# Kernel tuning notes

Hardware: AMD Instinct MI355X
Metric: run time of the kernel (lower is better)

The kernel has to match this reference:

```python
import jax, jax.numpy as jnp
import numpy as np

T, B, F = 197, 64, 768      # tokens (hardcoded 197 in module), batch, width
N, K = 8, 2                 # num_experts, top-k
CAP = int(197 * 1.0 * K / N)  # capacity = 49
H = 4 * F                   # expert hidden (c_fc out)
G = F // 4                  # gate hidden


def setup_inputs() -> dict:
    key = jax.random.key(0)
    ks = jax.random.split(key, 9)
    s = 0.02
    return {
        "x":   jax.random.normal(ks[0], (T, B, F), jnp.float32),
        # gate: Linear(F, F/4) -> ReLU -> Linear(F/4, N)
        "Wg1": jax.random.normal(ks[1], (F, G), jnp.float32) * s,
        "bg1": jnp.zeros((G,), jnp.float32),
        "Wg2": jax.random.normal(ks[2], (G, N), jnp.float32) * s,
        "bg2": jnp.zeros((N,), jnp.float32),
        # experts: per-expert Linear(F, 4F) -> ReLU -> Linear(4F, F), stacked over N
        "W1":  jax.random.normal(ks[3], (N, F, H), jnp.float32) * s,
        "b1":  jnp.zeros((N, H), jnp.float32),
        "W2":  jax.random.normal(ks[4], (N, H, F), jnp.float32) * s,
        "b2":  jnp.zeros((N, F), jnp.float32),
    }


def reference(x, Wg1, bg1, Wg2, bg2, W1, b1, W2, b2):
    # gating: softmax over experts (dim=2)
    logits = jax.nn.relu(x @ Wg1 + bg1) @ Wg2 + bg2          # [T,B,N]
    gw = jax.nn.softmax(logits, axis=2)                      # [T,B,N]

    # dense all-expert MLP (as-written: every expert on every token)
    h = jax.nn.relu(jnp.einsum('tbf,nfh->tbnh', x, W1) + b1)  # [T,B,N,H]
    eo = jnp.einsum('tbnh,nhf->tbnf', h, W2) + b2             # [T,B,N,F]

    # top-k expert mask (dim=2)
    _, idx = jax.lax.top_k(gw, K)                             # [T,B,K]
    mask_exp = jnp.any(jnp.arange(N)[None, None, None, :] == idx[..., None], axis=2)
    cw = gw * mask_exp                                        # [T,B,N]

    # capacity mask: top-CAP tokens per (batch, expert) along dim 0
    cwT = jnp.moveaxis(cw, 0, -1)                             # [B,N,T]
    _, idx2 = jax.lax.top_k(cwT, CAP)                         # [B,N,CAP]
    mask_cap = jnp.any(jnp.arange(T)[None, None, None, :] == idx2[..., None], axis=2)  # [B,N,T]
    fw = cw * jnp.moveaxis(mask_cap, -1, 0)                   # [T,B,N]

    # combine selected expert outputs, residual-style subtract
    out = jnp.einsum('tbnf,tbn->tbf', eo, fw) - x             # [T,B,F]
    return out
```

## Files before the change

kernel.cpp:

```cpp
#include <hip/hip_runtime.h>
#include <hip/hip_bf16.h>
#include <math.h>
#include <stdint.h>

#define T_ 197
#define B_ 64
#define F_ 768
#define N_ 8
#define CAP_ 49
#define H_ 3072
#define G_ 192
#define TB_ (T_*B_)
#define NBN_ (B_*N_)
#define ME_ 3200
#define MR_ 3136
#define MT_ 25600
#define KH_ 4
#define HCF_ 384
#define NPF_ 8

using bf16x8 = __attribute__((ext_vector_type(8))) short;
using f32x4  = __attribute__((ext_vector_type(4))) float;

__device__ __forceinline__ unsigned short f2bf(float v) {
    __hip_bfloat16 h = __float2bfloat16(v);
    return __builtin_bit_cast(unsigned short, h);
}
__device__ __forceinline__ float bf2f(unsigned short u) {
    unsigned int w = ((unsigned int)u) << 16;
    return __builtin_bit_cast(float, w);
}

#define GLL16(g, l) __builtin_amdgcn_global_load_lds( \
    (const __attribute__((address_space(1))) unsigned int*)(uintptr_t)(g), \
    (__attribute__((address_space(3))) unsigned int*)(uintptr_t)(l), 16, 0, 0)

__device__ __forceinline__ int xcd_swz(int bid, int nblk) {
    int q = nblk >> 3, r = nblk & 7;
    int xcd = bid & 7, idx = bid >> 3;
    int base = (xcd < r) ? xcd * (q + 1) : r * (q + 1) + (xcd - r) * q;
    return base + idx;
}

__global__ void k_init_out(const float* __restrict__ x, float* __restrict__ out) {
    int i = blockIdx.x * blockDim.x + threadIdx.x;
    const float4* xv = (const float4*)x;
    float4* ov = (float4*)out;
    float4 v = xv[i];
    ov[i] = make_float4(-v.x, -v.y, -v.z, -v.w);
}

__global__ __launch_bounds__(256) void k_gate1(
        const float* __restrict__ x, const float* __restrict__ Wg1,
        float* __restrict__ gs_part) {
    __shared__ float xs[64][35];
    __shared__ float wt[64][35];
    int bid = blockIdx.x;
    int bm = bid % 197; int rest = bid / 197;
    int bn = rest % 3, kh = rest / 3;
    int m0 = bm * 64, n0 = bn * 64, k0 = kh * (F_ / KH_);
    int tid = threadIdx.x;
    int tc = tid & 15, tr = tid >> 4;
    float acc[4][4] = {};

    int xr0 = tid >> 3, xc4 = (tid & 7) << 2;
    int wnn = tid & 63, wkw = tid >> 6;

    float4 xreg[2];
    float4 wreg[2];

    auto loadRegs = [&](int t) {
        int kb = k0 + t * 32;
        #pragma unroll
        for (int i = 0; i < 2; ++i) {
            int r = xr0 + i * 32;
            xreg[i] = *(const float4*)(x + (size_t)(m0 + r) * F_ + kb + xc4);
        }
        #pragma unroll
        for (int i = 0; i < 2; ++i) {
            int kkg = (wkw * 2 + i) * 4;
            const float* wp = Wg1 + (size_t)(kb + kkg) * G_ + n0 + wnn;
            wreg[i].x = wp[0];
            wreg[i].y = wp[G_];
            wreg[i].z = wp[2 * G_];
            wreg[i].w = wp[3 * G_];
        }
    };
    auto writeLDS = [&]() {
        #pragma unroll
        for (int i = 0; i < 2; ++i)
            *(float4*)&xs[xr0 + i * 32][xc4] = xreg[i];
        #pragma unroll
        for (int i = 0; i < 2; ++i)
            *(float4*)&wt[wnn][(wkw * 2 + i) * 4] = wreg[i];
    };

    loadRegs(0);
    for (int t = 0; t < 6; ++t) {
        __syncthreads();
        writeLDS();
        __syncthreads();
        if (t < 5) loadRegs(t + 1);
        #pragma unroll
        for (int kq = 0; kq < 8; ++kq) {
            float4 a[4], b[4];
            #pragma unroll
            for (int i = 0; i < 4; ++i) a[i] = *(const float4*)&xs[tr * 4 + i][kq * 4];
            #pragma unroll
            for (int j = 0; j < 4; ++j) b[j] = *(const float4*)&wt[tc + 16 * j][kq * 4];
            #pragma unroll
            for (int i = 0; i < 4; ++i)
                #pragma unroll
                for (int j = 0; j < 4; ++j)
                    acc[i][j] += a[i].x * b[j].x + a[i].y * b[j].y + a[i].z * b[j].z + a[i].w * b[j].w;
        }
    }
    float* gp = gs_part + (size_t)kh * TB_ * G_;
    #pragma unroll
    for (int j = 0; j < 4; ++j) {
        int c = n0 + tc + 16 * j;
        #pragma unroll
        for (int i = 0; i < 4; ++i) {
            int r = m0 + tr * 4 + i;
            gp[(size_t)r * G_ + c] = acc[i][j];
        }
    }
}

__global__ __launch_bounds__(256) void k_gate2(
        const float* __restrict__ gs_part, const float* __restrict__ bg1,
        const float* __restrict__ Wg2, const float* __restrict__ bg2,
        float* __restrict__ cw, int* __restrict__ ecnt) {
    __shared__ float gsh[32][200];
    __shared__ float wg2s[G_ * N_];
    __shared__ float lg[32][8];
    int tid = threadIdx.x;
    int id0 = blockIdx.x * 32;

    for (int i = tid; i < 32 * 48; i += 256) {
        int r = i / 48, c4 = i % 48;
        const float* p0 = gs_part + (size_t)(id0 + r) * G_ + c4 * 4;
        float4 a = *(const float4*)p0;
        float4 b = *(const float4*)(p0 + (size_t)TB_ * G_);
        float4 c = *(const float4*)(p0 + 2 * (size_t)TB_ * G_);
        float4 d = *(const float4*)(p0 + 3 * (size_t)TB_ * G_);
        float4 g = *(const float4*)(bg1 + c4 * 4);
        float4 v;
        v.x = fmaxf(a.x + b.x + c.x + d.x + g.x, 0.f);
        v.y = fmaxf(a.y + b.y + c.y + d.y + g.y, 0.f);
        v.z = fmaxf(a.z + b.z + c.z + d.z + g.z, 0.f);
        v.w = fmaxf(a.w + b.w + c.w + d.w + g.w, 0.f);
        ((float4*)&gsh[r][0])[c4] = v;
    }
    for (int i = tid; i < G_ * N_; i += 256) wg2s[i] = Wg2[i];
    __syncthreads();

    int tk = tid >> 3, n = tid & 7;
    float a = bg2[n];
    for (int k = 0; k < G_; ++k) a += gsh[tk][k] * wg2s[k * N_ + n];
    lg[tk][n] = a;
    __syncthreads();

    if (tid < 32) {
        int tk2 = tid;
        float p[8];
        float m = lg[tk2][0];
        #pragma unroll
        for (int nn = 1; nn < 8; ++nn) m = fmaxf(m, lg[tk2][nn]);
        float s = 0.f;
        #pragma unroll
        for (int nn = 0; nn < 8; ++nn) { p[nn] = expf(lg[tk2][nn] - m); s += p[nn]; }
        float inv = 1.f / s;
        #pragma unroll
        for (int nn = 0; nn < 8; ++nn) p[nn] *= inv;
        int i1 = 0; float v1 = p[0];
        #pragma unroll
        for (int nn = 1; nn < 8; ++nn) if (p[nn] > v1) { v1 = p[nn]; i1 = nn; }
        int i2 = -1; float v2 = -1.f;
        #pragma unroll
        for (int nn = 0; nn < 8; ++nn) if (nn != i1 && p[nn] > v2) { v2 = p[nn]; i2 = nn; }
        int id = id0 + tk2;
        int t = id / B_, b = id % B_;
        ecnt[id] = 0;
        #pragma unroll
        for (int nn = 0; nn < 8; ++nn) {
            float v = (nn == i1 || nn == i2) ? p[nn] : 0.f;
            cw[((size_t)(b * N_ + nn)) * T_ + t] = v;
        }
    }
}

__global__ __launch_bounds__(256) void k_gate(
        const float* __restrict__ x, const float* __restrict__ Wg1,
        const float* __restrict__ bg1, const float* __restrict__ Wg2,
        const float* __restrict__ bg2, float* __restrict__ cw,
        int* __restrict__ ecnt) {
    __shared__ float xsh[8][F_];
    __shared__ float gsl[8][G_];
    __shared__ float lg[8][N_];
    int tid = threadIdx.x;
    int id0 = blockIdx.x * 8;

    int gid = blockIdx.x * 256 + tid;
    if (gid < TB_ && ecnt) ecnt[gid] = 0;

    const float4* xv = (const float4*)(x + (size_t)id0 * F_);
    float4* xshv = (float4*)&xsh[0][0];
    for (int idx = tid; idx < 8 * (F_/4); idx += 256) xshv[idx] = xv[idx];
    __syncthreads();

    if (tid < G_) {
        float acc[8];
        float bb = bg1[tid];
        #pragma unroll
        for (int tk = 0; tk < 8; ++tk) acc[tk] = bb;
        for (int k = 0; k < F_; ++k) {
            float w = Wg1[k * G_ + tid];
            #pragma unroll
            for (int tk = 0; tk < 8; ++tk) acc[tk] += xsh[tk][k] * w;
        }
        #pragma unroll
        for (int tk = 0; tk < 8; ++tk) gsl[tk][tid] = fmaxf(acc[tk], 0.f);
    }
    __syncthreads();

    if (tid < 64) {
        int tk = tid >> 3, n = tid & 7;
        float acc = bg2[n];
        for (int k = 0; k < G_; ++k) acc += gsl[tk][k] * Wg2[k * N_ + n];
        lg[tk][n] = acc;
    }
    __syncthreads();

    if (tid < 8) {
        int tk = tid;
        float p[8];
        float m = lg[tk][0];
        #pragma unroll
        for (int n = 1; n < 8; ++n) m = fmaxf(m, lg[tk][n]);
        float s = 0.f;
        #pragma unroll
        for (int n = 0; n < 8; ++n) { p[n] = expf(lg[tk][n] - m); s += p[n]; }
        float inv = 1.f / s;
        #pragma unroll
        for (int n = 0; n < 8; ++n) p[n] *= inv;
        int i1 = 0; float v1 = p[0];
        #pragma unroll
        for (int n = 1; n < 8; ++n) if (p[n] > v1) { v1 = p[n]; i1 = n; }
        int i2 = -1; float v2 = -1.f;
        #pragma unroll
        for (int n = 0; n < 8; ++n) if (n != i1 && p[n] > v2) { v2 = p[n]; i2 = n; }
        int id = id0 + tk;
        int t = id / B_, b = id % B_;
        #pragma unroll
        for (int n = 0; n < 8; ++n) {
            float v = (n == i1 || n == i2) ? p[n] : 0.f;
            cw[((size_t)(b * N_ + n)) * T_ + t] = v;
        }
    }
}

__global__ __launch_bounds__(256) void k_capacity(
        const float* __restrict__ cw, int* __restrict__ toks,
        float* __restrict__ wts, int* __restrict__ counts,
        int* __restrict__ ecnt, int* __restrict__ erow) {
    __shared__ float v[T_];
    __shared__ int keep[T_];
    int tid = threadIdx.x;
    int bn = blockIdx.x;
    int b = bn >> 3, n = bn & 7;
    if (tid < T_) v[tid] = cw[(size_t)bn * T_ + tid];
    __syncthreads();
    int kp = 0; float my = 0.f;
    if (tid < T_) {
        my = v[tid];
        int rank = 0;
        for (int t2 = 0; t2 < T_; ++t2) {
            float vt = v[t2];
            rank += (vt > my) || (vt == my && t2 < tid);
        }
        kp = (rank < CAP_) && (my > 0.f);
    }
    if (tid < T_) keep[tid] = kp;
    __syncthreads();
    if (tid < T_ && kp) {
        int slot = 0;
        for (int t2 = 0; t2 < T_; ++t2) slot += (t2 < tid) ? keep[t2] : 0;
        toks[bn * CAP_ + slot] = tid;
        wts[bn * CAP_ + slot] = my;
        if (ecnt) {
            int orow = tid * B_ + b;
            int pos = atomicAdd(&ecnt[orow], 1);
            erow[orow * 2 + pos] = n * ME_ + b * CAP_ + slot;
        }
    }
    if (tid == 0) {
        int tot = 0;
        for (int t2 = 0; t2 < T_; ++t2) tot += keep[t2];
        counts[bn] = tot;
    }
}

__global__ __launch_bounds__(256) void k_repack(
        const float* __restrict__ W, unsigned short* __restrict__ WT, int K, int J) {
    __shared__ float tile[64][65];
    int bid = blockIdx.x;
    int nk = K >> 6, nj = J >> 6;
    int kt = bid % nk; bid /= nk;
    int jt = bid % nj; int e = bid / nj;
    int k0 = kt * 64, j0 = jt * 64;
    int tid = threadIdx.x;
    int jr = (tid & 15) << 2;
    int kr = tid >> 4;
    const float* src = W + ((size_t)e * K + k0) * J + j0;
    #pragma unroll
    for (int i = 0; i < 4; ++i) {
        float4 v = *(const float4*)(src + (size_t)(kr + 16 * i) * J + jr);
        *(float4*)&tile[kr + 16 * i][jr] = v;
    }
    __syncthreads();
    int c = tid & 7;
    int jrow = tid >> 3;
    #pragma unroll
    for (int i = 0; i < 2; ++i) {
        int j = jrow + 32 * i;
        float f[8];
        #pragma unroll
        for (int s = 0; s < 8; ++s) f[s] = tile[c * 8 + s][j];
        uint4 u;
        u.x = f2bf(f[0]) | ((unsigned)f2bf(f[1]) << 16);
        u.y = f2bf(f[2]) | ((unsigned)f2bf(f[3]) << 16);
        u.z = f2bf(f[4]) | ((unsigned)f2bf(f[5]) << 16);
        u.w = f2bf(f[6]) | ((unsigned)f2bf(f[7]) << 16);
        int jg = j0 + j;
        char* drow = (char*)WT + ((size_t)e * J + jg) * (size_t)K * 2 + (size_t)(k0 >> 6) * 128;
        *(uint4*)(drow + ((c << 4) ^ ((jg & 7) << 4))) = u;
    }
}

__global__ __launch_bounds__(256) void k_gather(
        const float* __restrict__ x, const int* __restrict__ toks,
        const int* __restrict__ counts, unsigned short* __restrict__ Xg) {
    int gi = blockIdx.x * 256 + threadIdx.x;
    int R = gi / 96, c = gi - R * 96;
    int e = R / ME_, re = R - e * ME_;
    uint4 val = make_uint4(0u, 0u, 0u, 0u);
    if (re < MR_) {
        int g = re / CAP_, slot = re - g * CAP_;
        int bn = g * N_ + e;
        if (slot < counts[bn]) {
            int t = toks[bn * CAP_ + slot];
            const float* xp = x + ((size_t)t * B_ + g) * F_ + c * 8;
            float4 v0 = *(const float4*)xp;
            float4 v1 = *(const float4*)(xp + 4);
            val.x = f2bf(v0.x) | ((unsigned)f2bf(v0.y) << 16);
            val.y = f2bf(v0.z) | ((unsigned)f2bf(v0.w) << 16);
            val.z = f2bf(v1.x) | ((unsigned)f2bf(v1.y) << 16);
            val.w = f2bf(v1.z) | ((unsigned)f2bf(v1.w) << 16);
        }
    }
    int w = (c * 16) & 127;
    char* dst = (char*)Xg + (size_t)R * 1536 + (c >> 3) * 128 + (w ^ ((R & 7) << 4));
    *(uint4*)dst = val;
}

__global__ __launch_bounds__(256) void k_gemm1(
        const unsigned short* __restrict__ W1T, const unsigned short* __restrict__ Xg,
        const float* __restrict__ b1, unsigned short* __restrict__ Hg,
        int e0, int nblk) {
    __shared__ char ldsA[2][16384];
    __shared__ char ldsB[2][16384];
    int swzb = xcd_swz(blockIdx.x, nblk);
    int mt = swzb / 24;
    int jt = swzb % 24;
    int em = mt / 25;
    int e = e0 + em;
    int tid = threadIdx.x, lane = tid & 63, wid = tid >> 6;
    int lr8 = lane >> 3, sl = (lane & 7) << 4;
    const char* Ab = (const char*)W1T + ((size_t)e * H_ + (size_t)jt * 128) * (F_ * 2);
    const char* Bb = (const char*)Xg + ((size_t)e * ME_ + (size_t)(mt % 25) * 128) * (F_ * 2);
    f32x4 acc[4][4] = {};
    int swz = (lane & 7) << 4;
    int q16 = (lane >> 4) << 4;

    auto stage = [&](int buf, int it) {
        int kb = it << 7;
        #pragma unroll
        for (int i = 0; i < 4; ++i) {
            int lr = wid * 32 + i * 8 + lr8;
            GLL16(Ab + (size_t)lr * 1536 + kb + sl, ldsA[buf] + (wid * 32 + i * 8) * 128);
            GLL16(Bb + (size_t)lr * 1536 + kb + sl, ldsB[buf] + (wid * 32 + i * 8) * 128);
        }
    };

    stage(0, 0);
    __syncthreads();
    int cur = 0;
    for (int it = 0; it < 12; ++it) {
        if (it < 11) stage(cur ^ 1, it + 1);
        const char* la = ldsA[cur] + ((wid & 1) * 64) * 128;
        const char* lb = ldsB[cur] + ((wid >> 1) * 64) * 128;
        #pragma unroll
        for (int ks = 0; ks < 2; ++ks) {
            bf16x8 af[4], bfr[4];
            int kk = (ks * 64 + q16) ^ swz;
            #pragma unroll
            for (int t = 0; t < 4; ++t) {
                int ro = (16 * t + (lane & 15)) * 128;
                af[t]  = *(const bf16x8*)(la + ro + kk);
                bfr[t] = *(const bf16x8*)(lb + ro + kk);
            }
            #pragma unroll
            for (int ti = 0; ti < 4; ++ti)
                #pragma unroll
                for (int tm = 0; tm < 4; ++tm)
                    acc[ti][tm] = __builtin_amdgcn_mfma_f32_16x16x32_bf16(af[ti], bfr[tm], acc[ti][tm], 0, 0, 0);
        }
        __syncthreads();
        cur ^= 1;
    }
    int jl0 = jt * 128 + (wid & 1) * 64;
    int ml0 = mt * 128 + (wid >> 1) * 64;
    const float* b1p = b1 + (size_t)e * H_;
    #pragma unroll
    for (int tj = 0; tj < 4; ++tj) {
        int jc = jl0 + 16 * tj + ((lane >> 4) << 2);
        float bb0 = b1p[jc], bb1 = b1p[jc + 1], bb2 = b1p[jc + 2], bb3 = b1p[jc + 3];
        #pragma unroll
        for (int tm = 0; tm < 4; ++tm) {
            int m = ml0 + 16 * tm + (lane & 15);
            f32x4 a = acc[tj][tm];
            unsigned int u0 = f2bf(fmaxf(a[0] + bb0, 0.f)) | ((unsigned)f2bf(fmaxf(a[1] + bb1, 0.f)) << 16);
            unsigned int u1 = f2bf(fmaxf(a[2] + bb2, 0.f)) | ((unsigned)f2bf(fmaxf(a[3] + bb3, 0.f)) << 16);
            int w = (jc * 2) & 127;
            char* dst = (char*)Hg + (size_t)m * (H_ * 2) + ((jc * 2) & ~127) + (w ^ ((m & 7) << 4));
            *(uint2*)dst = make_uint2(u0, u1);
        }
    }
}

__global__ __launch_bounds__(256) void k_gemm2(
        const unsigned short* __restrict__ W2T, const unsigned short* __restrict__ Hg,
        const float* __restrict__ b2, const float* __restrict__ wts,
        const int* __restrict__ counts, unsigned short* __restrict__ Og,
        int e0, int nblk) {
    __shared__ char ldsA[2][16384];
    __shared__ char ldsB[2][16384];
    int swzb = xcd_swz(blockIdx.x, nblk);
    int mt = swzb / 6;
    int ft = swzb % 6;
    int em = mt / 25;
    int e = e0 + em;
    int tid = threadIdx.x, lane = tid & 63, wid = tid >> 6;
    int lr8 = lane >> 3, sl = (lane & 7) << 4;
    const char* Ab = (const char*)W2T + ((size_t)e * F_ + (size_t)ft * 128) * (H_ * 2);
    const char* Bb = (const char*)Hg + (size_t)mt * 128 * (H_ * 2);
    f32x4 acc[4][4] = {};
    int swz = (lane & 7) << 4;
    int q16 = (lane >> 4) << 4;

    auto stage = [&](int buf, int it) {
        int kb = it << 7;
        #pragma unroll
        for (int i = 0; i < 4; ++i) {
            int lr = wid * 32 + i * 8 + lr8;
            GLL16(Ab + (size_t)lr * 6144 + kb + sl, ldsA[buf] + (wid * 32 + i * 8) * 128);
            GLL16(Bb + (size_t)lr * 6144 + kb + sl, ldsB[buf] + (wid * 32 + i * 8) * 128);
        }
    };

    stage(0, 0);
    __syncthreads();
    int cur = 0;
    for (int it = 0; it < 48; ++it) {
        if (it < 47) stage(cur ^ 1, it + 1);
        const char* la = ldsA[cur] + ((wid & 1) * 64) * 128;
        const char* lb = ldsB[cur] + ((wid >> 1) * 64) * 128;
        #pragma unroll
        for (int ks = 0; ks < 2; ++ks) {
            bf16x8 af[4], bfr[4];
            int kk = (ks * 64 + q16) ^ swz;
            #pragma unroll
            for (int t = 0; t < 4; ++t) {
                int ro = (16 * t + (lane & 15)) * 128;
                af[t]  = *(const bf16x8*)(la + ro + kk);
                bfr[t] = *(const bf16x8*)(lb + ro + kk);
            }
            #pragma unroll
            for (int ti = 0; ti < 4; ++ti)
                #pragma unroll
                for (int tm = 0; tm < 4; ++tm)
                    acc[ti][tm] = __builtin_amdgcn_mfma_f32_16x16x32_bf16(af[ti], bfr[tm], acc[ti][tm], 0, 0, 0);
        }
        __syncthreads();
        cur ^= 1;
    }
    int fl0 = ft * 128 + (wid & 1) * 64;
    int ml0 = mt * 128 + (wid >> 1) * 64;
    const float* b2p = b2 + (size_t)e * F_;
    float fwv[4]; int mrow[4];
    #pragma unroll
    for (int tm = 0; tm < 4; ++tm) {
        int m = ml0 + 16 * tm + (lane & 15);
        int re = m - em * ME_;
        float fw = 0.f;
        if (re < MR_) {
            int g = re / CAP_;
            int slot = re - g * CAP_;
            int bn = g * N_ + e;
            if (slot < counts[bn]) fw = wts[bn * CAP_ + slot];
        }
        fwv[tm] = fw;
        mrow[tm] = e0 * ME_ + m;
    }
    #pragma unroll
    for (int tf = 0; tf < 4; ++tf) {
        int f = fl0 + 16 * tf + ((lane >> 4) << 2);
        float c0 = b2p[f], c1 = b2p[f + 1], c2 = b2p[f + 2], c3 = b2p[f + 3];
        #pragma unroll
        for (int tm = 0; tm < 4; ++tm) {
            f32x4 a = acc[tf][tm];
            float fw = fwv[tm];
            unsigned int u0 = f2bf(fw * (a[0] + c0)) | ((unsigned)f2bf(fw * (a[1] + c1)) << 16);
            unsigned int u1 = f2bf(fw * (a[2] + c2)) | ((unsigned)f2bf(fw * (a[3] + c3)) << 16);
            *(uint2*)((char*)Og + (size_t)mrow[tm] * (F_ * 2) + f * 2) = make_uint2(u0, u1);
        }
    }
}

__global__ __launch_bounds__(256) void k_combine(
        const float* __restrict__ x, const unsigned short* __restrict__ Og,
        const int* __restrict__ ecnt, const int* __restrict__ erow,
        float* __restrict__ out) {
    int idx = blockIdx.x * 256 + threadIdx.x;
    int row = idx / 192, c4 = idx - row * 192;
    float4 s = make_float4(0.f, 0.f, 0.f, 0.f);
    int c = ecnt[row];
    if (c > 0) {
        ushort4 u = *(const ushort4*)(Og + (size_t)erow[row * 2] * F_ + c4 * 4);
        s.x += bf2f(u.x); s.y += bf2f(u.y); s.z += bf2f(u.z); s.w += bf2f(u.w);
    }
    if (c > 1) {
        ushort4 u = *(const ushort4*)(Og + (size_t)erow[row * 2 + 1] * F_ + c4 * 4);
        s.x += bf2f(u.x); s.y += bf2f(u.y); s.z += bf2f(u.z); s.w += bf2f(u.w);
    }
    float4 xv = ((const float4*)x)[idx];
    ((float4*)out)[idx] = make_float4(s.x - xv.x, s.y - xv.y, s.z - xv.z, s.w - xv.w);
}

__global__ __launch_bounds__(HCF_) void k_fc1(
        const float* __restrict__ x, const float* __restrict__ W1,
        const float* __restrict__ b1, const int* __restrict__ toks,
        const int* __restrict__ counts, __hip_bfloat16* __restrict__ h, int pass) {
    __shared__ float xs[25][F_];
    int tid = threadIdx.x;
    int bn = blockIdx.x >> 1;
    int half = blockIdx.x & 1;
    int r0 = half * 25;
    int b = bn >> 3, n = bn & 7;
    int c = counts[bn];
    for (int idx = tid; idx < 25 * (F_/4); idx += HCF_) {
        int r = idx / (F_/4), k4 = idx % (F_/4);
        int gr = r0 + r;
        float4 val = make_float4(0.f, 0.f, 0.f, 0.f);
        if (gr < c) {
            int t = toks[bn * CAP_ + gr];
            val = ((const float4*)(x + ((size_t)(t * B_ + b)) * F_))[k4];
        }
        ((float4*)&xs[r][0])[k4] = val;
    }
    __syncthreads();
    int j = pass * HCF_ + tid;
    const float* w1p = W1 + (size_t)n * F_ * H_ + j;
    float bias = b1[n * H_ + j];
    float acc[25];
    #pragma unroll
    for (int r = 0; r < 25; ++r) acc[r] = bias;
    const float4* xsv = (const float4*)&xs[0][0];
    for (int k4 = 0; k4 < F_/4; ++k4) {
        float w0 = w1p[(size_t)(4*k4+0) * H_];
        float w1v = w1p[(size_t)(4*k4+1) * H_];
        float w2v = w1p[(size_t)(4*k4+2) * H_];
        float w3v = w1p[(size_t)(4*k4+3) * H_];
        #pragma unroll
        for (int r = 0; r < 25; ++r) {
            float4 xv = xsv[r * (F_/4) + k4];
            acc[r] += xv.x*w0 + xv.y*w1v + xv.z*w2v + xv.w*w3v;
        }
    }
    __hip_bfloat16* hp = h + ((size_t)bn * CAP_ + r0) * HCF_ + tid;
    #pragma unroll
    for (int r = 0; r < 25; ++r) {
        int gr = r0 + r;
        if (gr < CAP_) hp[(size_t)r * HCF_] = __float2bfloat16(fmaxf(acc[r], 0.f));
    }
}

__global__ __launch_bounds__(768) void k_fc2(
        const float* __restrict__ W2, const float* __restrict__ b2,
        const int* __restrict__ toks, const float* __restrict__ wts,
        const int* __restrict__ counts, const __hip_bfloat16* __restrict__ h,
        float* __restrict__ out, int pass) {
    __shared__ float hs[CAP_][HCF_];
    int tid = threadIdx.x;
    int bn = blockIdx.x;
    int c = counts[bn];
    if (c == 0) return;
    int b = bn >> 3, n = bn & 7;
    const ushort4* hv = (const ushort4*)(h + (size_t)bn * CAP_ * HCF_);
    for (int idx = tid; idx < CAP_ * (HCF_/4); idx += 768) {
        ushort4 u = hv[idx];
        float4 fv;
        fv.x = __bfloat162float(*(const __hip_bfloat16*)&u.x);
        fv.y = __bfloat162float(*(const __hip_bfloat16*)&u.y);
        fv.z = __bfloat162float(*(const __hip_bfloat16*)&u.z);
        fv.w = __bfloat162float(*(const __hip_bfloat16*)&u.w);
        ((float4*)&hs[0][0])[idx] = fv;
    }
    __syncthreads();
    int f = tid;
    const float* w2p = W2 + (size_t)n * H_ * F_ + (size_t)(pass * HCF_) * F_ + f;
    float acc[CAP_];
    #pragma unroll
    for (int r = 0; r < CAP_; ++r) acc[r] = 0.f;
    for (int j4 = 0; j4 < HCF_/4; ++j4) {
        float w0 = w2p[(size_t)(4*j4+0) * F_];
        float w1v = w2p[(size_t)(4*j4+1) * F_];
        float w2v = w2p[(size_t)(4*j4+2) * F_];
        float w3v = w2p[(size_t)(4*j4+3) * F_];
        #pragma unroll
        for (int r = 0; r < CAP_; ++r) {
            float4 hh = ((const float4*)&hs[r][0])[j4];
            acc[r] += hh.x*w0 + hh.y*w1v + hh.z*w2v + hh.w*w3v;
        }
    }
    float bias = (pass == 0) ? b2[n * F_ + f] : 0.f;
    #pragma unroll
    for (int r = 0; r < CAP_; ++r) {
        if (r < c) {
            int t = toks[bn * CAP_ + r];
            float fw = wts[bn * CAP_ + r];
            atomicAdd(&out[((size_t)(t * B_ + b)) * F_ + f], fw * (acc[r] + bias));
        }
    }
}

extern "C" void kernel_launch(void* const* d_in, const int* in_sizes, int n_in,
                              void* d_out, int out_size, void* d_ws, size_t ws_size,
                              hipStream_t stream) {
    const float* x   = (const float*)d_in[0];
    const float* Wg1 = (const float*)d_in[1];
    const float* bg1 = (const float*)d_in[2];
    const float* Wg2 = (const float*)d_in[3];
    const float* bg2 = (const float*)d_in[4];
    const float* W1  = (const float*)d_in[5];
    const float* b1  = (const float*)d_in[6];
    const float* W2  = (const float*)d_in[7];
    const float* b2  = (const float*)d_in[8];
    float* out = (float*)d_out;

    size_t oW1T  = 0;
    size_t oW2T  = oW1T + (size_t)N_ * H_ * F_ * 2;
    size_t oXg   = oW2T + (size_t)N_ * H_ * F_ * 2;
    size_t oCw   = oXg  + (size_t)MT_ * F_ * 2;
    size_t oWts  = oCw  + (size_t)NBN_ * T_ * 4;
    size_t oTok  = oWts + (size_t)NBN_ * CAP_ * 4;
    size_t oCnt  = oTok + (size_t)NBN_ * CAP_ * 4;
    size_t oEcnt = oCnt + (size_t)NBN_ * 4;
    size_t oErow = oEcnt + (size_t)TB_ * 4;
    size_t oOg   = oErow + (size_t)TB_ * 8;
    size_t oHg   = oOg  + (size_t)MT_ * F_ * 2;
    size_t hgPerExpert = (size_t)ME_ * H_ * 2;

    int grp = 0;
    if (ws_size >= oHg + 8 * hgPerExpert) grp = 8;
    else if (ws_size >= oHg + 4 * hgPerExpert) grp = 4;
    else if (ws_size >= oHg + 2 * hgPerExpert) grp = 2;

    if (grp > 0) {
        unsigned short* W1T = (unsigned short*)((char*)d_ws + oW1T);
        unsigned short* W2T = (unsigned short*)((char*)d_ws + oW2T);
        unsigned short* Xg  = (unsigned short*)((char*)d_ws + oXg);
        unsigned short* Og  = (unsigned short*)((char*)d_ws + oOg);
        unsigned short* Hg  = (unsigned short*)((char*)d_ws + oHg);
        float* gs_part = (float*)((char*)d_ws + oHg);
        float* cw   = (float*)((char*)d_ws + oCw);
        float* wts  = (float*)((char*)d_ws + oWts);
        int* toks   = (int*)((char*)d_ws + oTok);
        int* counts = (int*)((char*)d_ws + oCnt);
        int* ecnt   = (int*)((char*)d_ws + oEcnt);
        int* erow   = (int*)((char*)d_ws + oErow);

        k_gate1<<<197 * 3 * KH_, 256, 0, stream>>>(x, Wg1, gs_part);
        k_gate2<<<TB_ / 32, 256, 0, stream>>>(gs_part, bg1, Wg2, bg2, cw, ecnt);
        k_capacity<<<NBN_, 256, 0, stream>>>(cw, toks, wts, counts, ecnt, erow);
        k_repack<<<N_ * (F_/64) * (H_/64), 256, 0, stream>>>(W1, W1T, F_, H_);
        k_repack<<<N_ * (H_/64) * (F_/64), 256, 0, stream>>>(W2, W2T, H_, F_);
        k_gather<<<(MT_ * 96) / 256, 256, 0, stream>>>(x, toks, counts, Xg);
        for (int e0 = 0; e0 < N_; e0 += grp) {
            int nblk1 = grp * 25 * 24;
            int nblk2 = grp * 25 * 6;
            k_gemm1<<<nblk1, 256, 0, stream>>>(W1T, Xg, b1, Hg, e0, nblk1);
            k_gemm2<<<nblk2, 256, 0, stream>>>(W2T, Hg, b2, wts, counts, Og, e0, nblk2);
        }
        k_combine<<<(TB_ * 192) / 256, 256, 0, stream>>>(x, Og, ecnt, erow, out);
    } else {
        __hip_bfloat16* h = (__hip_bfloat16*)d_ws;
        float* cw  = (float*)((char*)d_ws + (size_t)NBN_ * CAP_ * HCF_ * 2);
        float* wts = cw + (size_t)NBN_ * T_;
        int* toks  = (int*)(wts + NBN_ * CAP_);
        int* counts = toks + NBN_ * CAP_;
        k_init_out<<<(TB_ * F_) / 1024, 256, 0, stream>>>(x, out);
        k_gate<<<TB_ / 8, 256, 0, stream>>>(x, Wg1, bg1, Wg2, bg2, cw, nullptr);
        k_capacity<<<NBN_, 256, 0, stream>>>(cw, toks, wts, counts, nullptr, nullptr);
        for (int p = 0; p < NPF_; ++p) {
            k_fc1<<<NBN_ * 2, HCF_, 0, stream>>>(x, W1, b1, toks, counts, h, p);
            k_fc2<<<NBN_, 768, 0, stream>>>(W2, b2, toks, wts, counts, h, out, p);
        }
    }
}
```

Baseline: 513.3 us.

## Restructure gate GEMM tiling and stage GEMM epilogue stores through LDS

The gate1 kernel now computes all 192 gate columns per block with an outer-product register tile, so each x tile is loaded once instead of once per column block, and the Wg1 loads become coalesced float4 reads. The gemm1 and gemm2 epilogues write their bf16 results into an LDS tile first and then store full 16-byte row chunks to global memory, replacing scattered 8-byte stores. This removes redundant x traffic and uncoalesced writes, at the cost of an extra LDS round trip and sync. The gate kernel's larger per-thread accumulator tile may raise register pressure.

Result: no change. 507.2 us (-1.2%).

```diff
diff --git a/kernel.cpp b/kernel.cpp
--- a/kernel.cpp
+++ b/kernel.cpp
@@ -53,46 +53,41 @@
 __global__ __launch_bounds__(256) void k_gate1(
         const float* __restrict__ x, const float* __restrict__ Wg1,
         float* __restrict__ gs_part) {
-    __shared__ float xs[64][35];
-    __shared__ float wt[64][35];
-    int bid = blockIdx.x;
-    int bm = bid % 197; int rest = bid / 197;
-    int bn = rest % 3, kh = rest / 3;
-    int m0 = bm * 64, n0 = bn * 64, k0 = kh * (F_ / KH_);
-    int tid = threadIdx.x;
-    int tc = tid & 15, tr = tid >> 4;
-    float acc[4][4] = {};
-
-    int xr0 = tid >> 3, xc4 = (tid & 7) << 2;
-    int wnn = tid & 63, wkw = tid >> 6;
-
-    float4 xreg[2];
-    float4 wreg[2];
+    __shared__ float xs[32][68];
+    __shared__ float wt[32][200];
+    int bm = blockIdx.x % 197, kh = blockIdx.x / 197;
+    int m0 = bm * 64, k0 = kh * (F_ / KH_);
+    int tid = threadIdx.x, lane = tid & 63, wid = tid >> 6;
+    int mg = lane & 15;
+    int ng = (lane >> 4) + 4 * wid;
+    f32x4 acc[4][3] = {};
+
+    int xr = tid >> 3, xc = tid & 7;
+    float4 xreg0, xreg1;
+    float4 wreg[6];
 
     auto loadRegs = [&](int t) {
         int kb = k0 + t * 32;
-        #pragma unroll
-        for (int i = 0; i < 2; ++i) {
-            int r = xr0 + i * 32;
-            xreg[i] = *(const float4*)(x + (size_t)(m0 + r) * F_ + kb + xc4);
-        }
-        #pragma unroll
-        for (int i = 0; i < 2; ++i) {
-            int kkg = (wkw * 2 + i) * 4;
-            const float* wp = Wg1 + (size_t)(kb + kkg) * G_ + n0 + wnn;
-            wreg[i].x = wp[0];
-            wreg[i].y = wp[G_];
-            wreg[i].z = wp[2 * G_];
-            wreg[i].w = wp[3 * G_];
+        xreg0 = *(const float4*)(x + (size_t)(m0 + xr) * F_ + kb + xc * 4);
+        xreg1 = *(const float4*)(x + (size_t)(m0 + xr + 32) * F_ + kb + xc * 4);
+        #pragma unroll
+        for (int i = 0; i < 6; ++i) {
+            int idx = tid + i * 256;
+            int kr = idx / 48, nc = idx % 48;
+            wreg[i] = *(const float4*)(Wg1 + (size_t)(kb + kr) * G_ + nc * 4);
         }
     };
     auto writeLDS = [&]() {
-        #pragma unroll
-        for (int i = 0; i < 2; ++i)
-            *(float4*)&xs[xr0 + i * 32][xc4] = xreg[i];
-        #pragma unroll
-        for (int i = 0; i < 2; ++i)
-            *(float4*)&wt[wnn][(wkw * 2 + i) * 4] = wreg[i];
+        xs[xc * 4 + 0][xr] = xreg0.x;  xs[xc * 4 + 1][xr] = xreg0.y;
+        xs[xc * 4 + 2][xr] = xreg0.z;  xs[xc * 4 + 3][xr] = xreg0.w;
+        xs[xc * 4 + 0][xr + 32] = xreg1.x;  xs[xc * 4 + 1][xr + 32] = xreg1.y;
+        xs[xc * 4 + 2][xr + 32] = xreg1.z;  xs[xc * 4 + 3][xr + 32] = xreg1.w;
+        #pragma unroll
+        for (int i = 0; i < 6; ++i) {
+            int idx = tid + i * 256;
+            int kr = idx / 48, nc = idx % 48;
+            *(float4*)&wt[kr][nc * 4] = wreg[i];
+        }
     };
 
     loadRegs(0);
@@ -102,28 +97,30 @@
         __syncthreads();
         if (t < 5) loadRegs(t + 1);
         #pragma unroll
-        for (int kq = 0; kq < 8; ++kq) {
-            float4 a[4], b[4];
+        for (int k = 0; k < 32; ++k) {
+            float4 av = *(const float4*)&xs[k][mg * 4];
+            float4 b0 = *(const float4*)&wt[k][ng * 12];
+            float4 b1 = *(const float4*)&wt[k][ng * 12 + 4];
+            float4 b2 = *(const float4*)&wt[k][ng * 12 + 8];
+            float am[4] = {av.x, av.y, av.z, av.w};
             #pragma unroll
-            for (int i = 0; i < 4; ++i) a[i] = *(const float4*)&xs[tr * 4 + i][kq * 4];
-            #pragma unroll
-            for (int j = 0; j < 4; ++j) b[j] = *(const float4*)&wt[tc + 16 * j][kq * 4];
-            #pragma unroll
-            for (int i = 0; i < 4; ++i)
-                #pragma unroll
-                for (int j = 0; j < 4; ++j)
-                    acc[i][j] += a[i].x * b[j].x + a[i].y * b[j].y + a[i].z * b[j].z + a[i].w * b[j].w;
+            for (int mi = 0; mi < 4; ++mi) {
+                acc[mi][0][0] += am[mi] * b0.x; acc[mi][0][1] += am[mi] * b0.y;
+                acc[mi][0][2] += am[mi] * b0.z; acc[mi][0][3] += am[mi] * b0.w;
+                acc[mi][1][0] += am[mi] * b1.x; acc[mi][1][1] += am[mi] * b1.y;
+                acc[mi][1][2] += am[mi] * b1.z; acc[mi][1][3] += am[mi] * b1.w;
+                acc[mi][2][0] += am[mi] * b2.x; acc[mi][2][1] += am[mi] * b2.y;
+                acc[mi][2][2] += am[mi] * b2.z; acc[mi][2][3] += am[mi] * b2.w;
+            }
         }
     }
     float* gp = gs_part + (size_t)kh * TB_ * G_;
     #pragma unroll
-    for (int j = 0; j < 4; ++j) {
-        int c = n0 + tc + 16 * j;
-        #pragma unroll
-        for (int i = 0; i < 4; ++i) {
-            int r = m0 + tr * 4 + i;
-            gp[(size_t)r * G_ + c] = acc[i][j];
-        }
+    for (int mi = 0; mi < 4; ++mi) {
+        int r = m0 + mg * 4 + mi;
+        #pragma unroll
+        for (int jv = 0; jv < 3; ++jv)
+            *(f32x4*)(gp + (size_t)r * G_ + ng * 12 + jv * 4) = acc[mi][jv];
     }
 }
 
@@ -419,9 +416,10 @@
         __syncthreads();
         cur ^= 1;
     }
-    int jl0 = jt * 128 + (wid & 1) * 64;
-    int ml0 = mt * 128 + (wid >> 1) * 64;
-    const float* b1p = b1 + (size_t)e * H_;
+    char* tile = &ldsA[0][0];
+    int jl0 = (wid & 1) * 64;
+    int ml0 = (wid >> 1) * 64;
+    const float* b1p = b1 + (size_t)e * H_ + (size_t)jt * 128;
     #pragma unroll
     for (int tj = 0; tj < 4; ++tj) {
         int jc = jl0 + 16 * tj + ((lane >> 4) << 2);
@@ -432,10 +430,18 @@
             f32x4 a = acc[tj][tm];
             unsigned int u0 = f2bf(fmaxf(a[0] + bb0, 0.f)) | ((unsigned)f2bf(fmaxf(a[1] + bb1, 0.f)) << 16);
             unsigned int u1 = f2bf(fmaxf(a[2] + bb2, 0.f)) | ((unsigned)f2bf(fmaxf(a[3] + bb3, 0.f)) << 16);
-            int w = (jc * 2) & 127;
-            char* dst = (char*)Hg + (size_t)m * (H_ * 2) + ((jc * 2) & ~127) + (w ^ ((m & 7) << 4));
-            *(uint2*)dst = make_uint2(u0, u1);
-        }
+            int bcol = jc * 2;
+            int w = bcol & 127;
+            *(uint2*)(tile + m * 256 + (bcol & ~127) + (w ^ ((m & 7) << 4))) = make_uint2(u0, u1);
+        }
+    }
+    __syncthreads();
+    char* Hrow = (char*)Hg + (size_t)(mt * 128) * (H_ * 2) + (size_t)jt * 256;
+    #pragma unroll
+    for (int i = 0; i < 8; ++i) {
+        int idx = tid + i * 256;
+        int r = idx >> 4, c = (idx & 15) << 4;
+        *(uint4*)(Hrow + (size_t)r * (H_ * 2) + c) = *(const uint4*)(tile + r * 256 + c);
     }
 }
 
@@ -495,14 +501,15 @@
         __syncthreads();
         cur ^= 1;
     }
-    int fl0 = ft * 128 + (wid & 1) * 64;
-    int ml0 = mt * 128 + (wid >> 1) * 64;
-    const float* b2p = b2 + (size_t)e * F_;
-    float fwv[4]; int mrow[4];
+    char* tile = &ldsA[0][0];
+    int fl0 = (wid & 1) * 64;
+    int ml0 = (wid >> 1) * 64;
+    const float* b2p = b2 + (size_t)e * F_ + (size_t)ft * 128;
+    float fwv[4];
     #pragma unroll
     for (int tm = 0; tm < 4; ++tm) {
-        int m = ml0 + 16 * tm + (lane & 15);
-        int re = m - em * ME_;
+        int mloc = ml0 + 16 * tm + (lane & 15);
+        int re = mt * 128 + mloc - em * ME_;
         float fw = 0.f;
         if (re < MR_) {
             int g = re / CAP_;
@@ -511,20 +518,31 @@
             if (slot < counts[bn]) fw = wts[bn * CAP_ + slot];
         }
         fwv[tm] = fw;
-        mrow[tm] = e0 * ME_ + m;
     }
     #pragma unroll
     for (int tf = 0; tf < 4; ++tf) {
-        int f = fl0 + 16 * tf + ((lane >> 4) << 2);
-        float c0 = b2p[f], c1 = b2p[f + 1], c2 = b2p[f + 2], c3 = b2p[f + 3];
+        int fc = fl0 + 16 * tf + ((lane >> 4) << 2);
+        float c0 = b2p[fc], c1 = b2p[fc + 1], c2 = b2p[fc + 2], c3 = b2p[fc + 3];
         #pragma unroll
         for (int tm = 0; tm < 4; ++tm) {
+            int mloc = ml0 + 16 * tm + (lane & 15);
             f32x4 a = acc[tf][tm];
             float fw = fwv[tm];
             unsigned int u0 = f2bf(fw * (a[0] + c0)) | ((unsigned)f2bf(fw * (a[1] + c1)) << 16);
             unsigned int u1 = f2bf(fw * (a[2] + c2)) | ((unsigned)f2bf(fw * (a[3] + c3)) << 16);
-            *(uint2*)((char*)Og + (size_t)mrow[tm] * (F_ * 2) + f * 2) = make_uint2(u0, u1);
-        }
+            int bcol = fc * 2;
+            int w = bcol & 127;
+            *(uint2*)(tile + mloc * 256 + (bcol & ~127) + (w ^ ((mloc & 7) << 4))) = make_uint2(u0, u1);
+        }
+    }
+    __syncthreads();
+    char* Orow = (char*)Og + ((size_t)(e0 * ME_ + mt * 128)) * (F_ * 2) + (size_t)ft * 256;
+    #pragma unroll
+    for (int i = 0; i < 8; ++i) {
+        int idx = tid + i * 256;
+        int r = idx >> 4, c = (idx & 15) << 4;
+        const char* src = tile + r * 256 + (c & ~127) + ((c & 127) ^ ((r & 7) << 4));
+        *(uint4*)(Orow + (size_t)r * (F_ * 2) + c) = *(const uint4*)src;
     }
 }
 
@@ -691,7 +709,7 @@
         int* ecnt   = (int*)((char*)d_ws + oEcnt);
         int* erow   = (int*)((char*)d_ws + oErow);
 
-        k_gate1<<<197 * 3 * KH_, 256, 0, stream>>>(x, Wg1, gs_part);
+        k_gate1<<<197 * KH_, 256, 0, stream>>>(x, Wg1, gs_part);
         k_gate2<<<TB_ / 32, 256, 0, stream>>>(gs_part, bg1, Wg2, bg2, cw, ecnt);
         k_capacity<<<NBN_, 256, 0, stream>>>(cw, toks, wts, counts, ecnt, erow);
         k_repack<<<N_ * (F_/64) * (H_/64), 256, 0, stream>>>(W1, W1T, F_, H_);
```
